# Kernel optimization log

Hardware: AMD Instinct MI355X
Metric: run time of the kernel (lower is better)

## Reference

```python
import jax, jax.numpy as jnp
import numpy as np

IN_DIM = 512
HID = 1024
E = 16
TOPK = 2


def setup_inputs() -> dict:
    key = jax.random.key(0)
    ks = jax.random.split(key, 8)
    s = 0.02
    x = jax.random.normal(ks[0], (4, 2048, IN_DIM), dtype=jnp.float32)
    Wr = jax.random.normal(ks[1], (IN_DIM, E), dtype=jnp.float32) * s
    br = jnp.zeros((E,), dtype=jnp.float32)
    W1 = jax.random.normal(ks[2], (E, IN_DIM, HID), dtype=jnp.float32) * s
    b1 = jnp.zeros((E, HID), dtype=jnp.float32)
    W2 = jax.random.normal(ks[3], (E, HID, IN_DIM), dtype=jnp.float32) * s
    b2 = jnp.zeros((E, IN_DIM), dtype=jnp.float32)
    return {"x": x, "Wr": Wr, "br": br, "W1": W1, "b1": b1, "W2": W2, "b2": b2}


def reference(x, Wr, br, W1, b1, W2, b2):
    token_shape = x.shape[:-1]
    xf = x.reshape(-1, x.shape[-1])            # [T, D]
    T = xf.shape[0]

    # router (temperature = 1.0)
    logits = xf @ Wr + br                       # [T, E]
    probs = jax.nn.softmax(logits, axis=-1)
    topk_w, topk_idx = jax.lax.top_k(probs, TOPK)           # [T, K]
    topk_w = topk_w / jnp.maximum(topk_w.sum(-1, keepdims=True), 1e-9)

    # combine weights: [T, E], zero where not routed
    combine = jnp.zeros((T, E), dtype=xf.dtype).at[
        jnp.arange(T)[:, None], topk_idx].add(topk_w)

    # per-expert MLP (exact GELU, as torch nn.GELU default), weighted combine
    y = jnp.zeros_like(xf)
    for e in range(E):
        h = jax.nn.gelu(xf @ W1[e] + b1[e], approximate=False)  # [T, H]
        o = h @ W2[e] + b2[e]                                   # [T, D]
        y = y + combine[:, e:e + 1] * o

    # residual (in_dim == out_dim)
    y = xf + y
    return y.reshape(*token_shape, IN_DIM)
```

## Files before the change

kernel.cpp:

```cpp
#include <hip/hip_runtime.h>
#include <hip/hip_bf16.h>
#include <math.h>

#define IN_DIM 512
#define HID    1024
#define NE     16
#define T_TOK  8192
#define NPAIR  (T_TOK*2)

typedef __attribute__((ext_vector_type(8))) short bf16x8;
typedef __attribute__((ext_vector_type(8))) unsigned short ushort8;
typedef __attribute__((ext_vector_type(4))) float f32x4;

__device__ __forceinline__ unsigned short f2b(float f){
  unsigned u = __float_as_uint(f);
  u += 0x7FFF + ((u >> 16) & 1);
  return (unsigned short)(u >> 16);
}
__device__ __forceinline__ float b2f(unsigned short u){
  return __uint_as_float(((unsigned)u) << 16);
}

__device__ __forceinline__ void barrier_lds_only(){
  asm volatile("s_waitcnt lgkmcnt(0)" ::: "memory");
  __builtin_amdgcn_s_barrier();
}

__global__ __launch_bounds__(256) void fused_head(
    const float* __restrict__ x, const float* __restrict__ Wr, const float* __restrict__ br,
    unsigned short* __restrict__ xb, int* __restrict__ eid, float* __restrict__ pw,
    const float* __restrict__ W1, unsigned short* __restrict__ O1,
    const float* __restrict__ W2, unsigned short* __restrict__ O2)
{
  __shared__ __align__(16) char smraw[64*65*4];
  const int b = blockIdx.x;
  const int tid = threadIdx.x;

  if (b < 2048){
    float (*xs)[IN_DIM] = (float(*)[IN_DIM])smraw;
    int wid = tid >> 6, lane = tid & 63;
    int t = b*4 + wid;
    const float4* xr4 = (const float4*)(x + (size_t)t*IN_DIM);
    ushort4*      xb4 = (ushort4*)(xb + (size_t)t*IN_DIM);

    float4 v0 = xr4[lane];
    float4 v1 = xr4[64 + lane];
    ushort4 o0, o1;
    o0.x=f2b(v0.x); o0.y=f2b(v0.y); o0.z=f2b(v0.z); o0.w=f2b(v0.w);
    o1.x=f2b(v1.x); o1.y=f2b(v1.y); o1.z=f2b(v1.z); o1.w=f2b(v1.w);
    xb4[lane]      = o0;
    xb4[64 + lane] = o1;
    *(float4*)&xs[wid][lane*4]       = v0;
    *(float4*)&xs[wid][256 + lane*4] = v1;
    __syncthreads();

    const int qq = lane & 3, rsub = lane >> 2;
    float acc4[4] = {0.f, 0.f, 0.f, 0.f};
    #pragma unroll
    for (int j=0; j<32; j++){
      int row = j*16 + rsub;
      float xv = xs[wid][row];
      float4 w = *(const float4*)&Wr[(size_t)row*NE + qq*4];
      acc4[0] += xv*w.x; acc4[1] += xv*w.y;
      acc4[2] += xv*w.z; acc4[3] += xv*w.w;
    }
    #pragma unroll
    for (int off=4; off<64; off<<=1){
      #pragma unroll
      for (int i=0;i<4;i++) acc4[i] += __shfl_xor(acc4[i], off, 64);
    }
    float lg[16];
    #pragma unroll
    for (int q=0;q<4;q++){
      #pragma unroll
      for (int i=0;i<4;i++) lg[q*4+i] = __shfl(acc4[i], q, 64);
    }
    if (lane==0){
      #pragma unroll
      for (int i=0;i<NE;i++) lg[i] += br[i];
      int e0=0; float l0=lg[0];
      #pragma unroll
      for (int i=1;i<NE;i++) if (lg[i] > l0){ l0=lg[i]; e0=i; }
      int e1=-1; float l1=-3.0e38f;
      #pragma unroll
      for (int i=0;i<NE;i++) if (i!=e0 && lg[i] > l1){ l1=lg[i]; e1=i; }
      float w0 = 1.f/(1.f + __expf(l1 - l0));
      float w1 = 1.f - w0;
      pw[t*2+0] = w0; pw[t*2+1] = w1;
      eid[t*2+0] = e0; eid[t*2+1] = e1;
    }
    return;
  }

  float (*tile)[65] = (float(*)[65])smraw;
  const float* src; unsigned short* dst; int M, N, m0, n0;
  const int bb = b - 2048;
  if (bb < 2048){
    M = IN_DIM; N = HID;
    int e = bb >> 7, r = bb & 127;
    n0 = (r & 15)*64; m0 = (r >> 4)*64;
    src = W1 + (size_t)e*M*N; dst = O1 + (size_t)e*M*N;
  } else {
    int b2 = bb - 2048; M = HID; N = IN_DIM;
    int e = b2 >> 7, r = b2 & 127;
    n0 = (r & 7)*64; m0 = (r >> 3)*64;
    src = W2 + (size_t)e*M*N; dst = O2 + (size_t)e*M*N;
  }
  const int lr = tid >> 4, lc = (tid & 15)*4;
  #pragma unroll
  for (int i=0;i<4;i++)
    *(float4*)&tile[lr + i*16][lc] = *(const float4*)&src[(size_t)(m0 + lr + i*16)*N + n0 + lc];
  __syncthreads();
  const int nr = tid >> 3, mc = (tid & 7)*8;
  #pragma unroll
  for (int p=0;p<2;p++){
    int n = nr + p*32;
    ushort8 o;
    #pragma unroll
    for (int j=0;j<8;j++) o[j] = f2b(tile[mc+j][n]);
    *(ushort8*)&dst[(size_t)(n0 + n)*M + m0 + mc] = o;
  }
}

__global__ __launch_bounds__(1024) void bucket_kernel(const int* __restrict__ eid,
                                                      int* __restrict__ cnt,
                                                      int* __restrict__ bucket){
  int e = blockIdx.x;
  __shared__ int lbase;
  if (threadIdx.x == 0) lbase = 0;
  __syncthreads();
  int lane = threadIdx.x & 63, wid = threadIdx.x >> 6;
  int* be = bucket + e*T_TOK;
  for (int c = wid*64; c < NPAIR; c += 1024){
    int p = c + lane;
    bool ok = (eid[p] == e);
    unsigned long long m = __ballot(ok);
    int rank = __popcll(m & ((1ull << lane) - 1ull));
    int count = __popcll(m);
    int base = 0;
    if (lane == 0) base = atomicAdd(&lbase, count);
    base = __shfl(base, 0, 64);
    if (ok) be[base + rank] = p;
  }
  __syncthreads();
  if (threadIdx.x == 0) cnt[e] = lbase;
}

template<int KDIM, int NDIM, bool FIRST>
__global__ __launch_bounds__(256) void moe_gemm(
    const unsigned short* __restrict__ A,
    const unsigned short* __restrict__ Bm,
    const float* __restrict__ bias,
    const int* __restrict__ cnt,
    const int* __restrict__ bucket,
    const float* __restrict__ pw,
    unsigned short* __restrict__ hb,
    unsigned short* __restrict__ opb)
{
  constexpr int NS  = KDIM / 32;
  constexpr int NBT = NDIM / 128;

  int ntiles = 0;
  #pragma unroll
  for (int j=0;j<NE;j++) ntiles += ((cnt[j]+63)>>6)*NBT;

  __shared__ unsigned short As[2*64*32];
  __shared__ unsigned short Bs[2*128*32];

  int tid = threadIdx.x;
  int lane = tid & 63, wid = tid >> 6;
  int wm = (wid>>1)*32, wn = (wid&1)*64;
  int lr0 = tid >> 2;
  int c   = tid & 3;
  int sc  = (c ^ ((lr0 >> 1) & 3)) * 8;
  int wA  = lr0*32 + sc;
  int fr = lane & 15, fb = lane >> 4;
  int pf8 = (fb ^ ((fr >> 1) & 3)) * 8;
  int fq = (lane>>4)*4;

  const int t0 = (blockIdx.x & 7)*(gridDim.x >> 3) + (blockIdx.x >> 3);
  for (int t = t0; t < ntiles; t += gridDim.x){
    int e=0, tloc=0, ebase=0, ce=0, itl=1;
    {
      int cum=0, crow=0;
      #pragma unroll
      for (int j=0;j<NE;j++){
        int cj = cnt[j];
        int it = (cj+63)>>6;
        int tj = it * NBT;
        bool in = (t >= cum) & (t < cum+tj);
        if (in){ e=j; tloc=t-cum; ebase=crow; ce=cj; itl=it; }
        cum += tj; crow += cj;
      }
    }
    int i0 = (tloc % itl) * 64;
    int n0 = (tloc / itl) * 128;

    const int* buck = bucket + e*T_TOK;
    int posA = i0 + lr0;
    int arow;
    if (FIRST){
      int pair = (posA < ce) ? buck[posA] : buck[i0];
      arow = pair >> 1;
    } else {
      arow = ebase + posA;
      if (arow > NPAIR-1) arow = NPAIR-1;
    }
    const unsigned short* Ag = A + (size_t)arow*KDIM + c*8;
    const unsigned short* Bg = Bm + (size_t)e*NDIM*KDIM + (size_t)(n0 + lr0)*KDIM + c*8;

    f32x4 acc[2][4];
    #pragma unroll
    for (int a=0;a<2;a++)
      #pragma unroll
      for (int b2=0;b2<4;b2++)
        #pragma unroll
        for (int j=0;j<4;j++) acc[a][b2][j] = 0.f;

    float4 ar, br0, br1;
    ar  = *(const float4*)(Ag);
    br0 = *(const float4*)(Bg);
    br1 = *(const float4*)(Bg + (size_t)64*KDIM);
    *(float4*)(As + wA) = ar;
    *(float4*)(Bs + wA) = br0;
    *(float4*)(Bs + wA + 64*32) = br1;
    ar  = *(const float4*)(Ag + 32);
    br0 = *(const float4*)(Bg + 32);
    br1 = *(const float4*)(Bg + (size_t)64*KDIM + 32);
    barrier_lds_only();

    #pragma unroll 2
    for (int k = 0; k < NS; k++){
      const int cur = k & 1, nxt = cur ^ 1;
      float4 na, nb0, nb1;
      bool ld = (k + 2 < NS);
      if (ld){
        na  = *(const float4*)(Ag + (k+2)*32);
        nb0 = *(const float4*)(Bg + (k+2)*32);
        nb1 = *(const float4*)(Bg + (size_t)64*KDIM + (k+2)*32);
      }
      if (k + 1 < NS){
        *(float4*)(As + nxt*2048 + wA) = ar;
        *(float4*)(Bs + nxt*4096 + wA) = br0;
        *(float4*)(Bs + nxt*4096 + wA + 64*32) = br1;
      }
      if (ld){ ar = na; br0 = nb0; br1 = nb1; }

      const unsigned short* Ac = As + cur*2048;
      const unsigned short* Bc = Bs + cur*4096;
      bf16x8 af[2], bfr[4];
      #pragma unroll
      for (int s=0;s<2;s++) af[s]  = *(const bf16x8*)(Ac + (wm + s*16 + fr)*32 + pf8);
      #pragma unroll
      for (int u=0;u<4;u++) bfr[u] = *(const bf16x8*)(Bc + (wn + u*16 + fr)*32 + pf8);
      #pragma unroll
      for (int s=0;s<2;s++)
        #pragma unroll
        for (int u=0;u<4;u++)
          acc[s][u] = __builtin_amdgcn_mfma_f32_16x16x32_bf16(af[s], bfr[u], acc[s][u], 0,0,0);
      barrier_lds_only();
    }

    #pragma unroll
    for (int s=0;s<2;s++){
      #pragma unroll
      for (int i=0;i<4;i++){
        int row = wm + s*16 + fq + i;
        int pos = i0 + row;
        if (pos >= ce) continue;
        #pragma unroll
        for (int u=0;u<4;u++){
          int n = n0 + wn + u*16 + fr;
          float v = acc[s][u][i] + bias[e*NDIM + n];
          if (FIRST){
            float z2 = v*(1.5957691216057308f + 0.0713548162726009f*v*v);
            float g  = __fdividef(v, 1.f + __expf(-z2));
            hb[(size_t)(ebase + pos)*NDIM + n] = f2b(g);
          } else {
            int pair = buck[pos];
            opb[(size_t)pair*NDIM + n] = f2b(pw[pair]*v);
          }
        }
      }
    }
  }
}

__global__ __launch_bounds__(256) void combine_kernel(const float* __restrict__ x,
                                                      const unsigned short* __restrict__ opb,
                                                      float* __restrict__ out){
  int i = blockIdx.x*256 + threadIdx.x;
  int t  = i >> 7;
  int c4 = i & 127;
  float4 v = ((const float4*)x)[i];
  ushort4 a = ((const ushort4*)opb)[(size_t)(2*t)*128 + c4];
  ushort4 b = ((const ushort4*)opb)[(size_t)(2*t+1)*128 + c4];
  v.x += b2f(a.x) + b2f(b.x);
  v.y += b2f(a.y) + b2f(b.y);
  v.z += b2f(a.z) + b2f(b.z);
  v.w += b2f(a.w) + b2f(b.w);
  ((float4*)out)[i] = v;
}

extern "C" void kernel_launch(void* const* d_in, const int* in_sizes, int n_in,
                              void* d_out, int out_size, void* d_ws, size_t ws_size,
                              hipStream_t stream)
{
  const float* x  = (const float*)d_in[0];
  const float* Wr = (const float*)d_in[1];
  const float* br = (const float*)d_in[2];
  const float* W1 = (const float*)d_in[3];
  const float* b1 = (const float*)d_in[4];
  const float* W2 = (const float*)d_in[5];
  const float* b2 = (const float*)d_in[6];
  float* out = (float*)d_out;
  char* ws = (char*)d_ws;

  int*            cnt    = (int*)(ws + 0);
  int*            bucket = (int*)(ws + 1024);
  float*          pw     = (float*)(ws + 525312);
  unsigned short* xb     = (unsigned short*)(ws + 590848);
  unsigned short* w1t    = (unsigned short*)(ws + 8979456);
  unsigned short* w2t    = (unsigned short*)(ws + 25756672);
  unsigned short* hb     = (unsigned short*)(ws + 42533888);
  int*            eid    = (int*)(ws + 42533888);
  unsigned short* opb    = w1t;

  fused_head<<<6144, 256, 0, stream>>>(x, Wr, br, xb, eid, pw, W1, w1t, W2, w2t);
  bucket_kernel<<<NE, 1024, 0, stream>>>(eid, cnt, bucket);
  moe_gemm<IN_DIM, HID, true ><<<2176, 256, 0, stream>>>(
      xb, w1t, b1, cnt, bucket, pw, hb, opb);
  moe_gemm<HID, IN_DIM, false><<<1088, 256, 0, stream>>>(
      hb, w2t, b2, cnt, bucket, pw, hb, opb);
  combine_kernel<<<(T_TOK*IN_DIM/4)/256, 256, 0, stream>>>(x, opb, out);
}
```

Measured before the change: 233.2 us.

## Fuse expert bucketing into router head via global atomics, drop bucket kernel

Removes the separate bucket_kernel launch. Each routed token now appends its pair index directly into the per-expert bucket from the router head, using a global atomicAdd on padded per-expert counters. The counters are zeroed with a memset beforehand. This saves one launch and one pass over the eid array, at the cost of contended global atomics and a nondeterministic order of tokens within each bucket.

```diff
diff --git a/kernel.cpp b/kernel.cpp
--- a/kernel.cpp
+++ b/kernel.cpp
@@ -28,7 +28,8 @@
 
 __global__ __launch_bounds__(256) void fused_head(
     const float* __restrict__ x, const float* __restrict__ Wr, const float* __restrict__ br,
-    unsigned short* __restrict__ xb, int* __restrict__ eid, float* __restrict__ pw,
+    unsigned short* __restrict__ xb, int* __restrict__ cntp, int* __restrict__ bucket,
+    float* __restrict__ pw,
     const float* __restrict__ W1, unsigned short* __restrict__ O1,
     const float* __restrict__ W2, unsigned short* __restrict__ O2)
 {
@@ -75,19 +76,22 @@
       #pragma unroll
       for (int i=0;i<4;i++) lg[q*4+i] = __shfl(acc4[i], q, 64);
     }
+    #pragma unroll
+    for (int i=0;i<NE;i++) lg[i] += br[i];
+    int e0=0; float l0=lg[0];
+    #pragma unroll
+    for (int i=1;i<NE;i++) if (lg[i] > l0){ l0=lg[i]; e0=i; }
+    int e1=-1; float l1=-3.0e38f;
+    #pragma unroll
+    for (int i=0;i<NE;i++) if (i!=e0 && lg[i] > l1){ l1=lg[i]; e1=i; }
     if (lane==0){
-      #pragma unroll
-      for (int i=0;i<NE;i++) lg[i] += br[i];
-      int e0=0; float l0=lg[0];
-      #pragma unroll
-      for (int i=1;i<NE;i++) if (lg[i] > l0){ l0=lg[i]; e0=i; }
-      int e1=-1; float l1=-3.0e38f;
-      #pragma unroll
-      for (int i=0;i<NE;i++) if (i!=e0 && lg[i] > l1){ l1=lg[i]; e1=i; }
       float w0 = 1.f/(1.f + __expf(l1 - l0));
-      float w1 = 1.f - w0;
-      pw[t*2+0] = w0; pw[t*2+1] = w1;
-      eid[t*2+0] = e0; eid[t*2+1] = e1;
+      pw[t*2+0] = w0; pw[t*2+1] = 1.f - w0;
+    }
+    if (lane < 2){
+      int ee = (lane==0) ? e0 : e1;
+      int slot = atomicAdd(&cntp[ee*16], 1);
+      bucket[ee*T_TOK + slot] = t*2 + lane;
     }
     return;
   }
@@ -122,30 +126,6 @@
   }
 }
 
-__global__ __launch_bounds__(1024) void bucket_kernel(const int* __restrict__ eid,
-                                                      int* __restrict__ cnt,
-                                                      int* __restrict__ bucket){
-  int e = blockIdx.x;
-  __shared__ int lbase;
-  if (threadIdx.x == 0) lbase = 0;
-  __syncthreads();
-  int lane = threadIdx.x & 63, wid = threadIdx.x >> 6;
-  int* be = bucket + e*T_TOK;
-  for (int c = wid*64; c < NPAIR; c += 1024){
-    int p = c + lane;
-    bool ok = (eid[p] == e);
-    unsigned long long m = __ballot(ok);
-    int rank = __popcll(m & ((1ull << lane) - 1ull));
-    int count = __popcll(m);
-    int base = 0;
-    if (lane == 0) base = atomicAdd(&lbase, count);
-    base = __shfl(base, 0, 64);
-    if (ok) be[base + rank] = p;
-  }
-  __syncthreads();
-  if (threadIdx.x == 0) cnt[e] = lbase;
-}
-
 template<int KDIM, int NDIM, bool FIRST>
 __global__ __launch_bounds__(256) void moe_gemm(
     const unsigned short* __restrict__ A,
@@ -162,7 +142,7 @@
 
   int ntiles = 0;
   #pragma unroll
-  for (int j=0;j<NE;j++) ntiles += ((cnt[j]+63)>>6)*NBT;
+  for (int j=0;j<NE;j++) ntiles += ((cnt[j*16]+63)>>6)*NBT;
 
   __shared__ unsigned short As[2*64*32];
   __shared__ unsigned short Bs[2*128*32];
@@ -185,7 +165,7 @@
       int cum=0, crow=0;
       #pragma unroll
       for (int j=0;j<NE;j++){
-        int cj = cnt[j];
+        int cj = cnt[j*16];
         int it = (cj+63)>>6;
         int tj = it * NBT;
         bool in = (t >= cum) & (t < cum+tj);
@@ -323,11 +303,11 @@
   unsigned short* w1t    = (unsigned short*)(ws + 8979456);
   unsigned short* w2t    = (unsigned short*)(ws + 25756672);
   unsigned short* hb     = (unsigned short*)(ws + 42533888);
-  int*            eid    = (int*)(ws + 42533888);
   unsigned short* opb    = w1t;
 
-  fused_head<<<6144, 256, 0, stream>>>(x, Wr, br, xb, eid, pw, W1, w1t, W2, w2t);
-  bucket_kernel<<<NE, 1024, 0, stream>>>(eid, cnt, bucket);
+  hipMemsetAsync(cnt, 0, NE*16*sizeof(int), stream);
+
+  fused_head<<<6144, 256, 0, stream>>>(x, Wr, br, xb, cnt, bucket, pw, W1, w1t, W2, w2t);
   moe_gemm<IN_DIM, HID, true ><<<2176, 256, 0, stream>>>(
       xb, w1t, b1, cnt, bucket, pw, hb, opb);
   moe_gemm<HID, IN_DIM, false><<<1088, 256, 0, stream>>>(
```

Result: slower. 248.7 us (+6.6%).
